# Kernel tuning notes

Hardware: AMD Instinct MI355X
Metric: run time of the kernel (lower is better)

## Reference

```python
import jax, jax.numpy as jnp
import numpy as np

# Gemma3-style config
B, S, HID = 2, 2048, 2560      # 2 sequences of 2048 tokens (flattened ragged prefill, equal lengths)
H, KV, D = 8, 4, 256           # attention heads, kv heads (GQA groups=2), head_dim
WINDOW = 1024                  # sliding window (is_sliding=True)
EPS = 1e-6
SCALE = 256.0 ** -0.5          # query_pre_attn_scalar ** -0.5
ROPE_BASE = 10000.0            # rope_local_base_freq for sliding layers


def setup_inputs() -> dict:
    key = jax.random.key(0)
    ks = jax.random.split(key, 5)
    T = B * S
    hidden_states = jax.random.normal(ks[0], (T, HID), jnp.float32)
    # real rotary tables: positions restart per sequence
    inv_freq = 1.0 / (ROPE_BASE ** (np.arange(0, D, 2, dtype=np.float64) / D))  # [D/2]
    pos = np.tile(np.arange(S, dtype=np.float64), B)                             # [T]
    ang = pos[:, None] * inv_freq[None, :]                                       # [T, D/2]
    cos = jnp.asarray(np.cos(ang), jnp.float32)
    sin = jnp.asarray(np.sin(ang), jnp.float32)
    w_qkv = jax.random.normal(ks[1], ((H + 2 * KV) * D, HID), jnp.float32) * 0.02
    q_norm_w = 1.0 + jax.random.normal(ks[2], (D,), jnp.float32) * 0.02  # Gemma stores weight-1, loads +1
    k_norm_w = 1.0 + jax.random.normal(ks[3], (D,), jnp.float32) * 0.02
    w_o = jax.random.normal(ks[4], (HID, H * D), jnp.float32) * 0.02
    return dict(hidden_states=hidden_states, cos=cos, sin=sin, w_qkv=w_qkv,
                q_norm_w=q_norm_w, k_norm_w=k_norm_w, w_o=w_o)


def _rmsnorm(x, w):
    # per-head RMSNorm in fp32, as Gemma3FastRMSNorm. x: [T, h, D]
    xf = x.astype(jnp.float32)
    var = jnp.mean(xf * xf, axis=-1, keepdims=True)
    return (xf * jax.lax.rsqrt(var + EPS) * w).astype(x.dtype)


def _rope(x, cos, sin):
    # neox-style rotary: rotate across head_dim halves. x: [T, h, D]; cos/sin: [T, D/2]
    x1, x2 = x[..., : D // 2], x[..., D // 2:]
    c, s = cos[:, None, :], sin[:, None, :]
    return jnp.concatenate([x1 * c - x2 * s, x2 * c + x1 * s], axis=-1)


def reference(hidden_states, cos, sin, w_qkv, q_norm_w, k_norm_w, w_o):
    T = hidden_states.shape[0]
    qkv = hidden_states @ w_qkv.T                              # [T, (H+2KV)*D]
    q = qkv[:, : H * D].reshape(T, H, D)
    k = qkv[:, H * D: (H + KV) * D].reshape(T, KV, D)
    v = qkv[:, (H + KV) * D:].reshape(T, KV, D)
    q = _rmsnorm(q, q_norm_w)
    k = _rmsnorm(k, k_norm_w)
    q = _rope(q, cos, sin)
    k = _rope(k, cos, sin)
    # unflatten ragged tokens into [B, S, h, D] (equal-length prefill)
    qb = q.reshape(B, S, H, D)
    kb = jnp.repeat(k.reshape(B, S, KV, D), H // KV, axis=2)   # GQA expand
    vb = jnp.repeat(v.reshape(B, S, KV, D), H // KV, axis=2)
    scores = jnp.einsum('bqhd,bkhd->bhqk', qb, kb) * SCALE     # [B, H, S, S]
    i = jnp.arange(S)[:, None]
    j = jnp.arange(S)[None, :]
    mask = (j <= i) & ((i - j) < WINDOW)                       # causal + sliding window
    scores = jnp.where(mask, scores, jnp.float32(-1e30))
    p = jax.nn.softmax(scores, axis=-1)
    attn = jnp.einsum('bhqk,bkhd->bqhd', p, vb)                # [B, S, H, D]
    attn = attn.reshape(T, H * D)
    return attn @ w_o.T                                        # [T, HID]
```

## Files before the change

kernel.cpp:

```cpp
#include <hip/hip_runtime.h>
#include <cstdint>
#include <cstddef>

#define T_TOK 4096
#define HIDDIM 2560
#define NH 8
#define NKV 4
#define HD 256
#define SEQ 2048
#define NBATCH 2
#define WIN 1024
#define NQKV 4096
#define QSCALE 0.0625f

typedef unsigned short u16;
typedef __attribute__((ext_vector_type(8))) __bf16 bf16x8;
typedef __attribute__((ext_vector_type(8))) u16 u16x8;
typedef __attribute__((ext_vector_type(4))) float f32x4;

__device__ __forceinline__ u16 f2bf(float f) {
  union { float f; uint32_t u; } x{f};
  uint32_t r = x.u + 0x7FFFu + ((x.u >> 16) & 1u);
  return (u16)(r >> 16);
}
__device__ __forceinline__ float bf2f(u16 h) {
  union { uint32_t u; float f; } x{((uint32_t)h) << 16};
  return x.f;
}
__device__ __forceinline__ void gload_lds16(const void* g, void* l) {
  __builtin_amdgcn_global_load_lds((const __attribute__((address_space(1))) unsigned int*)g,
                                   (__attribute__((address_space(3))) unsigned int*)l, 16, 0, 0);
}
template <int N>
__device__ __forceinline__ void vmcnt_wait() {
  if constexpr (N >= 8) asm volatile("s_waitcnt vmcnt(8)" ::: "memory");
  else if constexpr (N == 6) asm volatile("s_waitcnt vmcnt(6)" ::: "memory");
  else if constexpr (N == 4) asm volatile("s_waitcnt vmcnt(4)" ::: "memory");
  else if constexpr (N == 3) asm volatile("s_waitcnt vmcnt(3)" ::: "memory");
  else asm volatile("s_waitcnt vmcnt(0)" ::: "memory");
}

__global__ void cvt_bf16(const float* __restrict__ in, u16* __restrict__ out, int n8) {
  int i = blockIdx.x * 256 + threadIdx.x;
  if (i >= n8) return;
  const f32x4* p = (const f32x4*)(in + (size_t)i * 8);
  f32x4 a = p[0], b = p[1];
  u16 o[8];
  o[0] = f2bf(a[0]); o[1] = f2bf(a[1]); o[2] = f2bf(a[2]); o[3] = f2bf(a[3]);
  o[4] = f2bf(b[0]); o[5] = f2bf(b[1]); o[6] = f2bf(b[2]); o[7] = f2bf(b[3]);
  *(u16x8*)(out + (size_t)i * 8) = *(const u16x8*)o;
}

template <int M, int N, int K, int BN, int OUTBF16>
__global__ __launch_bounds__(512, 2) void gemm256(const u16* __restrict__ A,
                                                  const u16* __restrict__ Bt,
                                                  void* __restrict__ Cp) {
  constexpr int NT = K / 32;
  constexpr int BCH = BN * 4;
  constexpr int LPT = (1024 + BCH) / 512;
  constexpr int NREP = BN / 64;
  constexpr int BUFB = 16384 + BN * 64;
  __shared__ char smem[4 * BUFB];

  const int tid = threadIdx.x, lane = tid & 63, w = tid >> 6;
  const int wr = w >> 2, wc = w & 3, hi = lane >> 4, lo = lane & 15;
  const int hi16 = hi * 16;
  constexpr int TOT = (M / 256) * (N / BN);
  const int bid = blockIdx.x;
  const int wg = (bid & 7) * (TOT / 8) + (bid >> 3);
  const int m0 = (wg / (N / BN)) * 256;
  const int n0 = (wg % (N / BN)) * BN;

  f32x4 acc[8][NREP] = {};

  auto stage = [&](int tt, int bb) {
    const int k0 = tt * 32;
    char* base = smem + bb * BUFB;
#pragma unroll
    for (int it = 0; it < 2; ++it) {
      int c = tid + it * 512;
      int r = (c >> 2) ^ ((c >> 4) & 1);
      int h = (c & 3) ^ (r & 3);
      gload_lds16(A + (size_t)(m0 + r) * K + k0 + h * 8, base + c * 16);
    }
#pragma unroll
    for (int it = 0; it < BCH / 512; ++it) {
      int c = tid + it * 512;
      int r = (c >> 2) ^ ((c >> 4) & 1);
      int h = (c & 3) ^ (r & 3);
      gload_lds16(Bt + (size_t)(n0 + r) * K + k0 + h * 8, base + 16384 + c * 16);
    }
  };
  auto body = [&](int bb) {
    char* base = smem + bb * BUFB;
    bf16x8 a[8], b[NREP];
#pragma unroll
    for (int mi = 0; mi < 8; ++mi) {
      int r = wr * 128 + mi * 16 + lo;
      a[mi] = *(const bf16x8*)(base + ((r * 64 + hi16) ^ ((r & 7) << 4)));
    }
#pragma unroll
    for (int ni = 0; ni < NREP; ++ni) {
      int r = wc * (BN / 4) + ni * 16 + lo;
      b[ni] = *(const bf16x8*)(base + 16384 + ((r * 64 + hi16) ^ ((r & 7) << 4)));
    }
    __builtin_amdgcn_s_setprio(1);
#pragma unroll
    for (int mi = 0; mi < 8; ++mi)
#pragma unroll
      for (int ni = 0; ni < NREP; ++ni)
        acc[mi][ni] = __builtin_amdgcn_mfma_f32_16x16x32_bf16(a[mi], b[ni], acc[mi][ni], 0, 0, 0);
    __builtin_amdgcn_s_setprio(0);
  };

  stage(0, 0); stage(1, 1); stage(2, 2);
  vmcnt_wait<2 * LPT>();
  __builtin_amdgcn_s_barrier();
  int t = 0;
  for (; t < NT - 3; ++t) {
    stage(t + 3, (t + 3) & 3);
    body(t & 3);
    vmcnt_wait<2 * LPT>();
    __builtin_amdgcn_s_barrier();
  }
  body(t & 3); vmcnt_wait<LPT>(); __builtin_amdgcn_s_barrier(); ++t;
  body(t & 3); vmcnt_wait<0>();   __builtin_amdgcn_s_barrier(); ++t;
  body(t & 3);

#pragma unroll
  for (int mi = 0; mi < 8; ++mi)
#pragma unroll
    for (int ni = 0; ni < NREP; ++ni) {
      int row = m0 + wr * 128 + mi * 16 + hi * 4;
      int col = n0 + wc * (BN / 4) + ni * 16 + lo;
#pragma unroll
      for (int r = 0; r < 4; ++r) {
        if (OUTBF16)
          ((u16*)Cp)[(size_t)(row + r) * N + col] = f2bf(acc[mi][ni][r]);
        else
          ((float*)Cp)[(size_t)(row + r) * N + col] = acc[mi][ni][r];
      }
    }
}

__global__ void norm_rope(const u16* __restrict__ qkv, const float* __restrict__ cosb,
                          const float* __restrict__ sinb, const float* __restrict__ qw,
                          const float* __restrict__ kw, u16* __restrict__ qn,
                          u16* __restrict__ kn) {
  int gw = blockIdx.x * 4 + (threadIdx.x >> 6);
  int lane = threadIdx.x & 63;
  int t = gw / 12, hh = gw % 12;
  const u16* x = qkv + (size_t)t * NQKV + hh * HD;
  int d = lane * 2;
  float x1a = bf2f(x[d]), x1b = bf2f(x[d + 1]);
  float x2a = bf2f(x[d + 128]), x2b = bf2f(x[d + 129]);
  float ss = x1a * x1a + x1b * x1b + x2a * x2a + x2b * x2b;
#pragma unroll
  for (int off = 1; off < 64; off <<= 1) ss += __shfl_xor(ss, off, 64);
  float inv = rsqrtf(ss * (1.0f / 256.0f) + 1e-6f);
  const float* wp = (hh < 8) ? qw : kw;
  float c0 = cosb[t * 128 + d], c1 = cosb[t * 128 + d + 1];
  float s0 = sinb[t * 128 + d], s1 = sinb[t * 128 + d + 1];
  float sc = (hh < 8) ? QSCALE : 1.0f;
  float y1a = x1a * inv * wp[d], y1b = x1b * inv * wp[d + 1];
  float y2a = x2a * inv * wp[d + 128], y2b = x2b * inv * wp[d + 129];
  float o1a = (y1a * c0 - y2a * s0) * sc, o1b = (y1b * c1 - y2b * s1) * sc;
  float o2a = (y2a * c0 + y1a * s0) * sc, o2b = (y2b * c1 + y1b * s1) * sc;
  u16* o = (hh < 8) ? (qn + ((size_t)t * 8 + hh) * HD) : (kn + ((size_t)t * 4 + (hh - 8)) * HD);
  ushort2 lo2, hi2;
  lo2.x = f2bf(o1a); lo2.y = f2bf(o1b);
  hi2.x = f2bf(o2a); hi2.y = f2bf(o2b);
  *(ushort2*)&o[d] = lo2;
  *(ushort2*)&o[d + 128] = hi2;
}

__global__ void vtransp(const u16* __restrict__ qkv, u16* __restrict__ vt) {
  const int b = blockIdx.y >> 2, kv = blockIdx.y & 3;
  const int s0 = blockIdx.x * 64;
  const int t = threadIdx.x;
  __shared__ u16 tile[64 * 64];
  for (int d0 = 0; d0 < 256; d0 += 64) {
#pragma unroll
    for (int it = 0; it < 2; ++it) {
      int c = t + it * 256;
      int sr = c >> 3, dc = (c & 7) * 8;
      bf16x8 v = *(const bf16x8*)&qkv[(size_t)(b * SEQ + s0 + sr) * NQKV + 3072 + kv * HD + d0 + dc];
      *(bf16x8*)((char*)tile + ((sr * 128 + dc * 2) ^ ((sr & 7) << 4))) = v;
    }
    __syncthreads();
#pragma unroll
    for (int it = 0; it < 2; ++it) {
      int c = t + it * 256;
      int dr = c >> 3, sc0 = (c & 7) * 8;
      union { u16 a[8]; bf16x8 v; } u;
#pragma unroll
      for (int j = 0; j < 8; ++j) {
        int s = sc0 + j;
        u.a[j] = *(const u16*)((char*)tile + ((s * 128 + dr * 2) ^ ((s & 7) << 4)));
      }
      *(bf16x8*)&vt[((size_t)(b * 4 + kv) * 256 + d0 + dr) * SEQ + s0 + sc0] = u.v;
    }
    __syncthreads();
  }
}

__global__ __launch_bounds__(256, 2) void attn_fwd(const u16* __restrict__ qn,
                                                   const u16* __restrict__ kn,
                                                   const u16* __restrict__ vt,
                                                   u16* __restrict__ aout) {
  const int qt = blockIdx.x * 64, h = blockIdx.y, b = blockIdx.z;
  const int kvh = h >> 1;
  const int t = threadIdx.x, lane = t & 63, w = t >> 6, hi = lane >> 4, lo = lane & 15;
  __shared__ u16 Ks[2][32 * 256];
  __shared__ u16 Vs[2][256 * 32];
  __shared__ u16 Ps[4][16 * 32];

  bf16x8 qf[8];
  const int qrow = qt + w * 16 + lo;
#pragma unroll
  for (int dd = 0; dd < 8; ++dd)
    qf[dd] = *(const bf16x8*)&qn[((size_t)(b * SEQ + qrow) * 8 + h) * HD + dd * 32 + hi * 8];

  f32x4 oacc[16] = {};
  float mrow[4] = {-3e38f, -3e38f, -3e38f, -3e38f};
  float lrow[4] = {0.f, 0.f, 0.f, 0.f};
  const int kstart = qt >= WIN ? qt - WIN : 0;
  const int irow = qt + w * 16 + hi * 4;

  auto stage = [&](int kt2, int bb) {
#pragma unroll
    for (int it = 0; it < 4; ++it) {
      int s = t + it * 256;
      int kr = s >> 5, ch = (s & 31) ^ (kr & 7);
      gload_lds16(kn + ((size_t)(b * SEQ + kt2 + kr) * 4 + kvh) * HD + ch * 8,
                  (char*)Ks[bb] + s * 16);
    }
#pragma unroll
    for (int it = 0; it < 4; ++it) {
      int s = t + it * 256;
      int rp = s >> 2;
      int dr = rp ^ ((rp >> 2) & 1);
      int ch = (s & 3) ^ (dr & 3);
      gload_lds16(vt + ((size_t)(b * 4 + kvh) * 256 + dr) * SEQ + kt2 + ch * 8,
                  (char*)Vs[bb] + s * 16);
    }
  };

  stage(kstart, 0);
  __syncthreads();
  int cur = 0;

  for (int kt = kstart; kt < qt + 64; kt += 32) {
    const bool more = (kt + 32) < (qt + 64);
    if (more) stage(kt + 32, cur ^ 1);
    f32x4 sacc[2];
#pragma unroll
    for (int kk = 0; kk < 2; ++kk) {
      f32x4 sa = {0.f, 0.f, 0.f, 0.f};
      int krow = kk * 16 + lo;
#pragma unroll
      for (int dd = 0; dd < 8; ++dd) {
        bf16x8 kf = *(const bf16x8*)((char*)Ks[cur] + ((krow * 512 + (dd * 32 + hi * 8) * 2) ^ ((krow & 7) << 4)));
        sa = __builtin_amdgcn_mfma_f32_16x16x32_bf16(qf[dd], kf, sa, 0, 0, 0);
      }
      sacc[kk] = sa;
    }
    float pe[2][4];
    float tmax[4] = {-3e38f, -3e38f, -3e38f, -3e38f};
#pragma unroll
    for (int kk = 0; kk < 2; ++kk)
#pragma unroll
      for (int r = 0; r < 4; ++r) {
        int i = irow + r, j = kt + kk * 16 + lo;
        bool ok = (j <= i) && (i - j < WIN);
        float sv = ok ? sacc[kk][r] : -3e38f;
        sacc[kk][r] = sv;
        tmax[r] = fmaxf(tmax[r], sv);
      }
#pragma unroll
    for (int off = 1; off < 16; off <<= 1)
#pragma unroll
      for (int r = 0; r < 4; ++r) tmax[r] = fmaxf(tmax[r], __shfl_xor(tmax[r], off, 64));
    float scl[4], tsum[4];
#pragma unroll
    for (int r = 0; r < 4; ++r) {
      float mnew = fmaxf(mrow[r], tmax[r]);
      scl[r] = __expf(mrow[r] - mnew);
      mrow[r] = mnew;
      tsum[r] = 0.f;
    }
#pragma unroll
    for (int kk = 0; kk < 2; ++kk)
#pragma unroll
      for (int r = 0; r < 4; ++r) {
        float sv = sacc[kk][r];
        float p = (sv <= -1e37f) ? 0.f : __expf(sv - mrow[r]);
        pe[kk][r] = p;
        tsum[r] += p;
      }
#pragma unroll
    for (int off = 1; off < 16; off <<= 1)
#pragma unroll
      for (int r = 0; r < 4; ++r) tsum[r] += __shfl_xor(tsum[r], off, 64);
#pragma unroll
    for (int r = 0; r < 4; ++r) lrow[r] = lrow[r] * scl[r] + tsum[r];
#pragma unroll
    for (int dt = 0; dt < 16; ++dt)
#pragma unroll
      for (int r = 0; r < 4; ++r) oacc[dt][r] *= scl[r];
#pragma unroll
    for (int kk = 0; kk < 2; ++kk)
#pragma unroll
      for (int r = 0; r < 4; ++r) {
        int q = hi * 4 + r, cc = kk * 16 + lo;
        *(u16*)((char*)&Ps[w][0] + ((q * 64 + cc * 2) ^ ((q & 7) << 4))) = f2bf(pe[kk][r]);
      }
    bf16x8 pf = *(const bf16x8*)((char*)&Ps[w][0] + ((lo * 64 + hi * 16) ^ ((lo & 7) << 4)));
#pragma unroll
    for (int dt = 0; dt < 16; ++dt) {
      int d = dt * 16 + lo;
      bf16x8 vf = *(const bf16x8*)((char*)Vs[cur] + ((d * 64 + hi * 16) ^ ((d & 7) << 4)));
      oacc[dt] = __builtin_amdgcn_mfma_f32_16x16x32_bf16(pf, vf, oacc[dt], 0, 0, 0);
    }
    __syncthreads();
    cur ^= 1;
  }
#pragma unroll
  for (int dt = 0; dt < 16; ++dt)
#pragma unroll
    for (int r = 0; r < 4; ++r) {
      int i = irow + r;
      aout[(size_t)(b * SEQ + i) * 2048 + h * HD + dt * 16 + lo] = f2bf(oacc[dt][r] / lrow[r]);
    }
}

extern "C" void kernel_launch(void* const* d_in, const int* in_sizes, int n_in,
                              void* d_out, int out_size, void* d_ws, size_t ws_size,
                              hipStream_t stream) {
  const float* hs = (const float*)d_in[0];
  const float* cosb = (const float*)d_in[1];
  const float* sinb = (const float*)d_in[2];
  const float* wqkv = (const float*)d_in[3];
  const float* qw = (const float*)d_in[4];
  const float* kw = (const float*)d_in[5];
  const float* wo = (const float*)d_in[6];
  char* ws = (char*)d_ws;
  u16* hs_b = (u16*)(ws);
  u16* wqkv_b = (u16*)(ws + 20971520);
  u16* wo_b = (u16*)(ws + 41943040);
  u16* qkv_b = (u16*)(ws + 52428800);
  u16* kn = (u16*)(ws + 85983232);
  u16* vt = (u16*)(ws + 94371840);
  u16* qn = wqkv_b;
  u16* attn = hs_b;

  cvt_bf16<<<5120, 256, 0, stream>>>(hs, hs_b, 1310720);
  cvt_bf16<<<5120, 256, 0, stream>>>(wqkv, wqkv_b, 1310720);
  cvt_bf16<<<2560, 256, 0, stream>>>(wo, wo_b, 655360);
  gemm256<4096, 4096, 2560, 256, 1><<<256, 512, 0, stream>>>(hs_b, wqkv_b, qkv_b);
  norm_rope<<<12288, 256, 0, stream>>>(qkv_b, cosb, sinb, qw, kw, qn, kn);
  vtransp<<<dim3(32, 8), 256, 0, stream>>>(qkv_b, vt);
  attn_fwd<<<dim3(32, 8, 2), 256, 0, stream>>>(qn, kn, vt, attn);
  gemm256<4096, 2560, 2048, 128, 0><<<320, 512, 0, stream>>>(attn, wo_b, d_out);
}
```

Before: 420.4 us.

## Fuse prep kernels, interleave GEMM loads with MFMA halves, skip interior attention masking

Merges the three fp32->bf16 conversion launches into one kernel and the norm/rope and V transpose kernels into one launch. The GEMM main loop is split so A and B tile loads are issued between two half-MFMA phases, with extra barriers. The attention softmax skips mask evaluation for key tiles that are fully inside the causal window. These changes target launch overhead and load/compute overlap. The extra barriers in the GEMM may add synchronization cost.

```diff
diff --git a/kernel.cpp b/kernel.cpp
--- a/kernel.cpp
+++ b/kernel.cpp
@@ -40,10 +40,15 @@
   else asm volatile("s_waitcnt vmcnt(0)" ::: "memory");
 }
 
-__global__ void cvt_bf16(const float* __restrict__ in, u16* __restrict__ out, int n8) {
+__global__ void cvt_all(const float* __restrict__ hs, const float* __restrict__ wqkv,
+                        const float* __restrict__ wo, u16* __restrict__ out) {
   int i = blockIdx.x * 256 + threadIdx.x;
-  if (i >= n8) return;
-  const f32x4* p = (const f32x4*)(in + (size_t)i * 8);
+  const float* src;
+  int off;
+  if (i < 1310720)      { src = hs;   off = i; }
+  else if (i < 2621440) { src = wqkv; off = i - 1310720; }
+  else                  { src = wo;   off = i - 2621440; }
+  const f32x4* p = (const f32x4*)(src + (size_t)off * 8);
   f32x4 a = p[0], b = p[1];
   u16 o[8];
   o[0] = f2bf(a[0]); o[1] = f2bf(a[1]); o[2] = f2bf(a[2]); o[3] = f2bf(a[3]);
@@ -73,7 +78,7 @@
 
   f32x4 acc[8][NREP] = {};
 
-  auto stage = [&](int tt, int bb) {
+  auto stageA = [&](int tt, int bb) {
     const int k0 = tt * 32;
     char* base = smem + bb * BUFB;
 #pragma unroll
@@ -83,6 +88,10 @@
       int h = (c & 3) ^ (r & 3);
       gload_lds16(A + (size_t)(m0 + r) * K + k0 + h * 8, base + c * 16);
     }
+  };
+  auto stageB = [&](int tt, int bb) {
+    const int k0 = tt * 32;
+    char* base = smem + bb * BUFB;
 #pragma unroll
     for (int it = 0; it < BCH / 512; ++it) {
       int c = tid + it * 512;
@@ -91,11 +100,13 @@
       gload_lds16(Bt + (size_t)(n0 + r) * K + k0 + h * 8, base + 16384 + c * 16);
     }
   };
-  auto body = [&](int bb) {
+
+  auto body = [&](int bb, int tt, int wmode) {
     char* base = smem + bb * BUFB;
     bf16x8 a[8], b[NREP];
-#pragma unroll
-    for (int mi = 0; mi < 8; ++mi) {
+    if (tt >= 0) stageA(tt, tt & 3);
+#pragma unroll
+    for (int mi = 0; mi < 4; ++mi) {
       int r = wr * 128 + mi * 16 + lo;
       a[mi] = *(const bf16x8*)(base + ((r * 64 + hi16) ^ ((r & 7) << 4)));
     }
@@ -104,28 +115,45 @@
       int r = wc * (BN / 4) + ni * 16 + lo;
       b[ni] = *(const bf16x8*)(base + 16384 + ((r * 64 + hi16) ^ ((r & 7) << 4)));
     }
+    __builtin_amdgcn_s_barrier();
     __builtin_amdgcn_s_setprio(1);
 #pragma unroll
-    for (int mi = 0; mi < 8; ++mi)
+    for (int mi = 0; mi < 4; ++mi)
 #pragma unroll
       for (int ni = 0; ni < NREP; ++ni)
         acc[mi][ni] = __builtin_amdgcn_mfma_f32_16x16x32_bf16(a[mi], b[ni], acc[mi][ni], 0, 0, 0);
     __builtin_amdgcn_s_setprio(0);
+    __builtin_amdgcn_s_barrier();
+    if (tt >= 0) stageB(tt, tt & 3);
+#pragma unroll
+    for (int mi = 4; mi < 8; ++mi) {
+      int r = wr * 128 + mi * 16 + lo;
+      a[mi] = *(const bf16x8*)(base + ((r * 64 + hi16) ^ ((r & 7) << 4)));
+    }
+    if (wmode == 0) vmcnt_wait<2 * LPT>();
+    else if (wmode == 1) vmcnt_wait<LPT>();
+    else vmcnt_wait<0>();
+    __builtin_amdgcn_s_barrier();
+    __builtin_amdgcn_s_setprio(1);
+#pragma unroll
+    for (int mi = 4; mi < 8; ++mi)
+#pragma unroll
+      for (int ni = 0; ni < NREP; ++ni)
+        acc[mi][ni] = __builtin_amdgcn_mfma_f32_16x16x32_bf16(a[mi], b[ni], acc[mi][ni], 0, 0, 0);
+    __builtin_amdgcn_s_setprio(0);
+    __builtin_amdgcn_s_barrier();
   };
 
-  stage(0, 0); stage(1, 1); stage(2, 2);
+  stageA(0, 0); stageB(0, 0);
+  stageA(1, 1); stageB(1, 1);
+  stageA(2, 2); stageB(2, 2);
   vmcnt_wait<2 * LPT>();
   __builtin_amdgcn_s_barrier();
   int t = 0;
-  for (; t < NT - 3; ++t) {
-    stage(t + 3, (t + 3) & 3);
-    body(t & 3);
-    vmcnt_wait<2 * LPT>();
-    __builtin_amdgcn_s_barrier();
-  }
-  body(t & 3); vmcnt_wait<LPT>(); __builtin_amdgcn_s_barrier(); ++t;
-  body(t & 3); vmcnt_wait<0>();   __builtin_amdgcn_s_barrier(); ++t;
-  body(t & 3);
+  for (; t < NT - 3; ++t) body(t & 3, t + 3, 0);
+  body(t & 3, -1, 1); ++t;
+  body(t & 3, -1, 2); ++t;
+  body(t & 3, -1, 2);
 
 #pragma unroll
   for (int mi = 0; mi < 8; ++mi)
@@ -143,64 +171,66 @@
     }
 }
 
-__global__ void norm_rope(const u16* __restrict__ qkv, const float* __restrict__ cosb,
-                          const float* __restrict__ sinb, const float* __restrict__ qw,
-                          const float* __restrict__ kw, u16* __restrict__ qn,
-                          u16* __restrict__ kn) {
-  int gw = blockIdx.x * 4 + (threadIdx.x >> 6);
-  int lane = threadIdx.x & 63;
-  int t = gw / 12, hh = gw % 12;
-  const u16* x = qkv + (size_t)t * NQKV + hh * HD;
-  int d = lane * 2;
-  float x1a = bf2f(x[d]), x1b = bf2f(x[d + 1]);
-  float x2a = bf2f(x[d + 128]), x2b = bf2f(x[d + 129]);
-  float ss = x1a * x1a + x1b * x1b + x2a * x2a + x2b * x2b;
-#pragma unroll
-  for (int off = 1; off < 64; off <<= 1) ss += __shfl_xor(ss, off, 64);
-  float inv = rsqrtf(ss * (1.0f / 256.0f) + 1e-6f);
-  const float* wp = (hh < 8) ? qw : kw;
-  float c0 = cosb[t * 128 + d], c1 = cosb[t * 128 + d + 1];
-  float s0 = sinb[t * 128 + d], s1 = sinb[t * 128 + d + 1];
-  float sc = (hh < 8) ? QSCALE : 1.0f;
-  float y1a = x1a * inv * wp[d], y1b = x1b * inv * wp[d + 1];
-  float y2a = x2a * inv * wp[d + 128], y2b = x2b * inv * wp[d + 129];
-  float o1a = (y1a * c0 - y2a * s0) * sc, o1b = (y1b * c1 - y2b * s1) * sc;
-  float o2a = (y2a * c0 + y1a * s0) * sc, o2b = (y2b * c1 + y1b * s1) * sc;
-  u16* o = (hh < 8) ? (qn + ((size_t)t * 8 + hh) * HD) : (kn + ((size_t)t * 4 + (hh - 8)) * HD);
-  ushort2 lo2, hi2;
-  lo2.x = f2bf(o1a); lo2.y = f2bf(o1b);
-  hi2.x = f2bf(o2a); hi2.y = f2bf(o2b);
-  *(ushort2*)&o[d] = lo2;
-  *(ushort2*)&o[d + 128] = hi2;
-}
-
-__global__ void vtransp(const u16* __restrict__ qkv, u16* __restrict__ vt) {
-  const int b = blockIdx.y >> 2, kv = blockIdx.y & 3;
-  const int s0 = blockIdx.x * 64;
-  const int t = threadIdx.x;
+__global__ void normvt(const u16* __restrict__ qkv, const float* __restrict__ cosb,
+                       const float* __restrict__ sinb, const float* __restrict__ qw,
+                       const float* __restrict__ kw, u16* __restrict__ qn,
+                       u16* __restrict__ kn, u16* __restrict__ vt) {
   __shared__ u16 tile[64 * 64];
-  for (int d0 = 0; d0 < 256; d0 += 64) {
-#pragma unroll
-    for (int it = 0; it < 2; ++it) {
-      int c = t + it * 256;
-      int sr = c >> 3, dc = (c & 7) * 8;
-      bf16x8 v = *(const bf16x8*)&qkv[(size_t)(b * SEQ + s0 + sr) * NQKV + 3072 + kv * HD + d0 + dc];
-      *(bf16x8*)((char*)tile + ((sr * 128 + dc * 2) ^ ((sr & 7) << 4))) = v;
-    }
-    __syncthreads();
-#pragma unroll
-    for (int it = 0; it < 2; ++it) {
-      int c = t + it * 256;
-      int dr = c >> 3, sc0 = (c & 7) * 8;
-      union { u16 a[8]; bf16x8 v; } u;
-#pragma unroll
-      for (int j = 0; j < 8; ++j) {
-        int s = sc0 + j;
-        u.a[j] = *(const u16*)((char*)tile + ((s * 128 + dr * 2) ^ ((s & 7) << 4)));
+  if (blockIdx.x < 12288) {
+    int gw = blockIdx.x * 4 + (threadIdx.x >> 6);
+    int lane = threadIdx.x & 63;
+    int t = gw / 12, hh = gw % 12;
+    const u16* x = qkv + (size_t)t * NQKV + hh * HD;
+    int d = lane * 2;
+    float x1a = bf2f(x[d]), x1b = bf2f(x[d + 1]);
+    float x2a = bf2f(x[d + 128]), x2b = bf2f(x[d + 129]);
+    float ss = x1a * x1a + x1b * x1b + x2a * x2a + x2b * x2b;
+#pragma unroll
+    for (int off = 1; off < 64; off <<= 1) ss += __shfl_xor(ss, off, 64);
+    float inv = rsqrtf(ss * (1.0f / 256.0f) + 1e-6f);
+    const float* wp = (hh < 8) ? qw : kw;
+    float c0 = cosb[t * 128 + d], c1 = cosb[t * 128 + d + 1];
+    float s0 = sinb[t * 128 + d], s1 = sinb[t * 128 + d + 1];
+    float sc = (hh < 8) ? QSCALE : 1.0f;
+    float y1a = x1a * inv * wp[d], y1b = x1b * inv * wp[d + 1];
+    float y2a = x2a * inv * wp[d + 128], y2b = x2b * inv * wp[d + 129];
+    float o1a = (y1a * c0 - y2a * s0) * sc, o1b = (y1b * c1 - y2b * s1) * sc;
+    float o2a = (y2a * c0 + y1a * s0) * sc, o2b = (y2b * c1 + y1b * s1) * sc;
+    u16* o = (hh < 8) ? (qn + ((size_t)t * 8 + hh) * HD) : (kn + ((size_t)t * 4 + (hh - 8)) * HD);
+    ushort2 lo2, hi2;
+    lo2.x = f2bf(o1a); lo2.y = f2bf(o1b);
+    hi2.x = f2bf(o2a); hi2.y = f2bf(o2b);
+    *(ushort2*)&o[d] = lo2;
+    *(ushort2*)&o[d + 128] = hi2;
+  } else {
+    int bid2 = blockIdx.x - 12288;
+    const int xb = bid2 & 31, yb = bid2 >> 5;
+    const int b = yb >> 2, kv = yb & 3;
+    const int s0 = xb * 64;
+    const int t = threadIdx.x;
+    for (int d0 = 0; d0 < 256; d0 += 64) {
+#pragma unroll
+      for (int it = 0; it < 2; ++it) {
+        int c = t + it * 256;
+        int sr = c >> 3, dc = (c & 7) * 8;
+        bf16x8 v = *(const bf16x8*)&qkv[(size_t)(b * SEQ + s0 + sr) * NQKV + 3072 + kv * HD + d0 + dc];
+        *(bf16x8*)((char*)tile + ((sr * 128 + dc * 2) ^ ((sr & 7) << 4))) = v;
       }
-      *(bf16x8*)&vt[((size_t)(b * 4 + kv) * 256 + d0 + dr) * SEQ + s0 + sc0] = u.v;
-    }
-    __syncthreads();
+      __syncthreads();
+#pragma unroll
+      for (int it = 0; it < 2; ++it) {
+        int c = t + it * 256;
+        int dr = c >> 3, sc0 = (c & 7) * 8;
+        union { u16 a[8]; bf16x8 v; } u;
+#pragma unroll
+        for (int j = 0; j < 8; ++j) {
+          int s = sc0 + j;
+          u.a[j] = *(const u16*)((char*)tile + ((s * 128 + dr * 2) ^ ((s & 7) << 4)));
+        }
+        *(bf16x8*)&vt[((size_t)(b * 4 + kv) * 256 + d0 + dr) * SEQ + s0 + sc0] = u.v;
+      }
+      __syncthreads();
+    }
   }
 }
 
@@ -265,18 +295,26 @@
       }
       sacc[kk] = sa;
     }
+    const bool needmask = (kt + 32 > qt) || (qt >= WIN && kt < kstart + 64);
     float pe[2][4];
     float tmax[4] = {-3e38f, -3e38f, -3e38f, -3e38f};
-#pragma unroll
-    for (int kk = 0; kk < 2; ++kk)
-#pragma unroll
-      for (int r = 0; r < 4; ++r) {
-        int i = irow + r, j = kt + kk * 16 + lo;
-        bool ok = (j <= i) && (i - j < WIN);
-        float sv = ok ? sacc[kk][r] : -3e38f;
-        sacc[kk][r] = sv;
-        tmax[r] = fmaxf(tmax[r], sv);
-      }
+    if (needmask) {
+#pragma unroll
+      for (int kk = 0; kk < 2; ++kk)
+#pragma unroll
+        for (int r = 0; r < 4; ++r) {
+          int i = irow + r, j = kt + kk * 16 + lo;
+          bool ok = (j <= i) && (i - j < WIN);
+          float sv = ok ? sacc[kk][r] : -3e38f;
+          sacc[kk][r] = sv;
+          tmax[r] = fmaxf(tmax[r], sv);
+        }
+    } else {
+#pragma unroll
+      for (int kk = 0; kk < 2; ++kk)
+#pragma unroll
+        for (int r = 0; r < 4; ++r) tmax[r] = fmaxf(tmax[r], sacc[kk][r]);
+    }
 #pragma unroll
     for (int off = 1; off < 16; off <<= 1)
 #pragma unroll
@@ -289,15 +327,26 @@
       mrow[r] = mnew;
       tsum[r] = 0.f;
     }
-#pragma unroll
-    for (int kk = 0; kk < 2; ++kk)
-#pragma unroll
-      for (int r = 0; r < 4; ++r) {
-        float sv = sacc[kk][r];
-        float p = (sv <= -1e37f) ? 0.f : __expf(sv - mrow[r]);
-        pe[kk][r] = p;
-        tsum[r] += p;
-      }
+    if (needmask) {
+#pragma unroll
+      for (int kk = 0; kk < 2; ++kk)
+#pragma unroll
+        for (int r = 0; r < 4; ++r) {
+          float sv = sacc[kk][r];
+          float p = (sv <= -1e37f) ? 0.f : __expf(sv - mrow[r]);
+          pe[kk][r] = p;
+          tsum[r] += p;
+        }
+    } else {
+#pragma unroll
+      for (int kk = 0; kk < 2; ++kk)
+#pragma unroll
+        for (int r = 0; r < 4; ++r) {
+          float p = __expf(sacc[kk][r] - mrow[r]);
+          pe[kk][r] = p;
+          tsum[r] += p;
+        }
+    }
 #pragma unroll
     for (int off = 1; off < 16; off <<= 1)
 #pragma unroll
@@ -354,12 +403,9 @@
   u16* qn = wqkv_b;
   u16* attn = hs_b;
 
-  cvt_bf16<<<5120, 256, 0, stream>>>(hs, hs_b, 1310720);
-  cvt_bf16<<<5120, 256, 0, stream>>>(wqkv, wqkv_b, 1310720);
-  cvt_bf16<<<2560, 256, 0, stream>>>(wo, wo_b, 655360);
+  cvt_all<<<12800, 256, 0, stream>>>(hs, wqkv, wo, (u16*)ws);
   gemm256<4096, 4096, 2560, 256, 1><<<256, 512, 0, stream>>>(hs_b, wqkv_b, qkv_b);
-  norm_rope<<<12288, 256, 0, stream>>>(qkv_b, cosb, sinb, qw, kw, qn, kn);
-  vtransp<<<dim3(32, 8), 256, 0, stream>>>(qkv_b, vt);
+  normvt<<<12544, 256, 0, stream>>>(qkv_b, cosb, sinb, qw, kw, qn, kn, vt);
   attn_fwd<<<dim3(32, 8, 2), 256, 0, stream>>>(qn, kn, vt, attn);
   gemm256<4096, 2560, 2048, 128, 0><<<320, 512, 0, stream>>>(attn, wo_b, d_out);
 }
```

Result: no change. 419.8 us (-0.1%).
